# Kernel tuning notes

Measured on AMD Instinct MI355X. Metric: run time of the kernel, lower is better.

## Reference

```python
import jax, jax.numpy as jnp
import numpy as np

NS = 48          # scalar channel multiplicity ('48x0e' input irreps)
NV = 10          # vector multiplicity ('10x1o' output irreps)
N = 20000        # nodes
E = 100000       # edges
W_NUMEL = NS * NS + NS * NV  # e3nn FullyConnectedTensorProduct weight_numel = 2784
OUT_DIM = NS + 3 * NV        # '48x0e + 10x1o' -> 78


def setup_inputs() -> dict:
    key = jax.random.key(0)
    ks = jax.random.split(key, 8)
    node_attr = jax.random.normal(ks[0], (N, NS), dtype=jnp.float32)
    edge_index = jax.random.randint(ks[1], (2, E), 0, N, dtype=jnp.int32)
    edge_attr = jax.random.normal(ks[2], (E, NS), dtype=jnp.float32)
    edge_sh = jax.random.normal(ks[3], (E, 9), dtype=jnp.float32)  # sh lmax=2: 1+3+5
    fc1_w = jax.random.normal(ks[4], (3 * NS, 3 * NS), dtype=jnp.float32) / np.float32(np.sqrt(3 * NS))
    fc1_b = jnp.zeros((3 * NS,), dtype=jnp.float32)
    fc2_w = jax.random.normal(ks[5], (3 * NS, W_NUMEL), dtype=jnp.float32) / np.float32(np.sqrt(3 * NS))
    fc2_b = jnp.zeros((W_NUMEL,), dtype=jnp.float32)
    return {"node_attr": node_attr, "edge_index": edge_index, "edge_attr": edge_attr,
            "edge_sh": edge_sh, "fc1_w": fc1_w, "fc1_b": fc1_b, "fc2_w": fc2_w, "fc2_b": fc2_b}


def reference(node_attr, edge_index, edge_attr, edge_sh, fc1_w, fc1_b, fc2_w, fc2_b):
    src, dst = edge_index[0], edge_index[1]
    # edge features = [edge_attr, src scalars, dst scalars]  (n_edge_features = 3*ns)
    ea = jnp.concatenate([edge_attr, node_attr[src, :NS], node_attr[dst, :NS]], axis=-1)
    # edge MLP -> per-edge tensor-product weights (shared_weights=False)
    h = jax.nn.relu(ea @ fc1_w + fc1_b)
    w = h @ fc2_w + fc2_b                      # [E, W_NUMEL]
    w0 = w[:, :NS * NS].reshape(E, NS, NS)     # path 0e x 0e -> 0e
    w1 = w[:, NS * NS:].reshape(E, NS, NV)     # path 0e x 1o -> 1o
    x = node_attr[dst]                         # gathered scalar node features [E, NS]
    sh0 = edge_sh[:, :1]                       # l=0 component [E,1]
    sh1 = edge_sh[:, 1:4]                      # l=1 components [E,3]
    norm = np.float32(1.0 / np.sqrt(NS))       # path fan-in normalization (mul1*mul2 = NS*1)
    out0 = jnp.einsum('ei,eik->ek', x, w0) * sh0 * norm                # [E, NS]
    out1 = jnp.einsum('ek,em->ekm', jnp.einsum('ei,eik->ek', x, w1), sh1) * norm  # [E, NV, 3]
    tp = jnp.concatenate([out0, out1.reshape(E, NV * 3)], axis=-1)     # [E, OUT_DIM]
    # scatter-mean to source nodes (reduce='mean', dim_size=N)
    summed = jax.ops.segment_sum(tp, src, num_segments=N)
    counts = jax.ops.segment_sum(jnp.ones((E, 1), tp.dtype), src, num_segments=N)
    return summed / jnp.maximum(counts, 1.0)
```

## Files before the change

kernel.cpp:

```cpp
#include <hip/hip_runtime.h>
#include <hip/hip_bf16.h>

#define NS_    48
#define NV_    10
#define N_NODE 20000
#define N_EDGE 100000
#define HID    144
#define OUTC   58
#define ODIM   78
#define TILE   64
#define LDE    160
#define WNUM   2784

typedef __attribute__((ext_vector_type(8))) short bf8;
typedef __attribute__((ext_vector_type(4))) float f32x4;

__device__ __forceinline__ short f2bf(float x) {
  __hip_bfloat16 h = __float2bfloat16(x);
  union { __hip_bfloat16 b; short s; } u; u.b = h; return u.s;
}

__global__ void prep_fc1(const float* __restrict__ w, short* __restrict__ dst) {
  int idx = blockIdx.x * 256 + threadIdx.x;
  if (idx >= 9 * 5 * 512) return;
  int j = idx & 7, l = (idx >> 3) & 63, t = idx >> 9;
  int ks = t % 5, nt = t / 5;
  int k = ks * 32 + ((l >> 4) << 3) + j;
  int n = nt * 16 + (l & 15);
  dst[idx] = f2bf(k < HID ? w[k * HID + n] : 0.f);
}

__global__ void prep_g(const float* __restrict__ w, const float* __restrict__ b,
                       short* __restrict__ dst) {
  int idx = blockIdx.x * 256 + threadIdx.x;
  if (idx >= 48 * 4 * 5 * 512) return;
  int j = idx & 7, l = (idx >> 3) & 63, t = idx >> 9;
  int ks = t % 5, u = t / 5;
  int strip = u & 3, i = u >> 2;
  int k = ks * 32 + ((l >> 4) << 3) + j;
  int c = strip * 16 + (l & 15);
  float v = 0.f;
  if (c < OUTC) {
    if (k < HID)
      v = (c < NS_) ? w[k * WNUM + i * NS_ + c]
                    : w[k * WNUM + NS_ * NS_ + i * NV_ + (c - NS_)];
    else if (k == HID)
      v = (c < NS_) ? b[i * NS_ + c]
                    : b[NS_ * NS_ + i * NV_ + (c - NS_)];
  }
  dst[idx] = f2bf(v);
}

__global__ __launch_bounds__(256, 4) void fused_edge(
    const float* __restrict__ node_attr, const int* __restrict__ eidx,
    const float* __restrict__ edge_attr, const float* __restrict__ edge_sh,
    const float* __restrict__ fc1_b,
    const short* __restrict__ gfrag, const short* __restrict__ fc1frag,
    float* __restrict__ out, int* __restrict__ counts)
{
  __shared__ short EA[TILE * LDE];
  __shared__ float xT[NS_ * TILE];
  __shared__ float shs[TILE * 4];
  __shared__ int   srcs[TILE];

  const int tid  = threadIdx.x;
  const int lane = tid & 63;
  const int wv   = tid >> 6;
  const int base = blockIdx.x * TILE;

  for (int t = tid; t < TILE * 16; t += 256) {
    int r = t >> 4, c = t & 15;
    EA[r * LDE + HID + c] = 0;
  }

  {
    const int el = tid >> 2, part = tid & 3;
    const int e  = base + el;
    const bool ev = e < N_EDGE;
    const int es = ev ? eidx[e] : 0;
    const int ed = ev ? eidx[N_EDGE + e] : 0;
    if (part == 0) {
      srcs[el] = es;
      #pragma unroll
      for (int c = 0; c < 4; ++c) shs[el * 4 + c] = ev ? edge_sh[(size_t)e * 9 + c] : 0.f;
    }
    const float4* pa = (const float4*)(edge_attr + (size_t)e * NS_);
    const float4* ps = (const float4*)(node_attr + (size_t)es * NS_);
    const float4* pd = (const float4*)(node_attr + (size_t)ed * NS_);
    const float4 z4 = make_float4(0.f, 0.f, 0.f, 0.f);
    #pragma unroll
    for (int q = 0; q < 3; ++q) {
      const int c0 = part * 12 + q * 4;
      float4 va = ev ? pa[part * 3 + q] : z4;
      float4 vs = ev ? ps[part * 3 + q] : z4;
      float4 vd = ev ? pd[part * 3 + q] : z4;
      EA[el * LDE + c0 + 0] = f2bf(va.x);
      EA[el * LDE + c0 + 1] = f2bf(va.y);
      EA[el * LDE + c0 + 2] = f2bf(va.z);
      EA[el * LDE + c0 + 3] = f2bf(va.w);
      EA[el * LDE + NS_ + c0 + 0] = f2bf(vs.x);
      EA[el * LDE + NS_ + c0 + 1] = f2bf(vs.y);
      EA[el * LDE + NS_ + c0 + 2] = f2bf(vs.z);
      EA[el * LDE + NS_ + c0 + 3] = f2bf(vs.w);
      EA[el * LDE + 2 * NS_ + c0 + 0] = f2bf(vd.x);
      EA[el * LDE + 2 * NS_ + c0 + 1] = f2bf(vd.y);
      EA[el * LDE + 2 * NS_ + c0 + 2] = f2bf(vd.z);
      EA[el * LDE + 2 * NS_ + c0 + 3] = f2bf(vd.w);
      xT[(c0 + 0) * TILE + el] = vd.x;
      xT[(c0 + 1) * TILE + el] = vd.y;
      xT[(c0 + 2) * TILE + el] = vd.z;
      xT[(c0 + 3) * TILE + el] = vd.w;
    }
  }
  __syncthreads();

  {
    const int mrow = lane & 15;
    const int koff = (lane >> 4) << 3;
    bf8 aF[5];
    #pragma unroll
    for (int ks = 0; ks < 5; ++ks)
      aF[ks] = *(const bf8*)&EA[(wv * 16 + mrow) * LDE + ks * 32 + koff];
    #pragma unroll
    for (int nt = 0; nt < 9; ++nt) {
      f32x4 acc = {0.f, 0.f, 0.f, 0.f};
      #pragma unroll
      for (int ks = 0; ks < 5; ++ks) {
        bf8 bF = *(const bf8*)&fc1frag[((nt * 5 + ks) * 64 + lane) * 8];
        acc = __builtin_amdgcn_mfma_f32_16x16x32_bf16(aF[ks], bF, acc, 0, 0, 0);
      }
      const int col = nt * 16 + mrow;
      const float bb = fc1_b[col];
      #pragma unroll
      for (int r = 0; r < 4; ++r) {
        float h = acc[r] + bb;
        h = h > 0.f ? h : 0.f;
        EA[(wv * 16 + ((lane >> 4) << 2) + r) * LDE + col] = f2bf(h);
      }
    }
    if (lane < 16) EA[(wv * 16 + lane) * LDE + HID] = (short)0x3F80;
  }
  __syncthreads();

  {
    const int mrow = lane & 15;
    const int koff = (lane >> 4) << 3;
    const int g0 = (lane >> 4) << 2;

    f32x4 oacc[4];
    #pragma unroll
    for (int mt = 0; mt < 4; ++mt) oacc[mt] = (f32x4){0.f, 0.f, 0.f, 0.f};

    bf8 aF[4][5];
    #pragma unroll
    for (int mt = 0; mt < 4; ++mt)
      #pragma unroll
      for (int ks = 0; ks < 5; ++ks)
        aF[mt][ks] = *(const bf8*)&EA[(mt * 16 + mrow) * LDE + ks * 32 + koff];

    for (int i = 0; i < NS_; ++i) {
      bf8 bF[5];
      #pragma unroll
      for (int ks = 0; ks < 5; ++ks)
        bF[ks] = *(const bf8*)&gfrag[(((i * 4 + wv) * 5 + ks) * 64 + lane) * 8];
      #pragma unroll
      for (int mt = 0; mt < 4; ++mt) {
        f32x4 wi = {0.f, 0.f, 0.f, 0.f};
        #pragma unroll
        for (int ks = 0; ks < 5; ++ks)
          wi = __builtin_amdgcn_mfma_f32_16x16x32_bf16(aF[mt][ks], bF[ks], wi, 0, 0, 0);
        const float4 xs = *(const float4*)&xT[i * TILE + mt * 16 + g0];
        oacc[mt][0] += xs.x * wi[0];
        oacc[mt][1] += xs.y * wi[1];
        oacc[mt][2] += xs.z * wi[2];
        oacc[mt][3] += xs.w * wi[3];
      }
    }

    const float nrm = 0.14433756729740643f;
    const int col = wv * 16 + mrow;
    #pragma unroll
    for (int mt = 0; mt < 4; ++mt) {
      #pragma unroll
      for (int r = 0; r < 4; ++r) {
        const int erow = mt * 16 + g0 + r;
        const int e = base + erow;
        if (e < N_EDGE) {
          const int s = srcs[erow];
          const float v = oacc[mt][r] * nrm;
          if (col < NS_) {
            atomicAdd(&out[s * ODIM + col], v * shs[erow * 4 + 0]);
          } else if (col < OUTC) {
            const int kp = col - NS_;
            atomicAdd(&out[s * ODIM + NS_ + kp * 3 + 0], v * shs[erow * 4 + 1]);
            atomicAdd(&out[s * ODIM + NS_ + kp * 3 + 1], v * shs[erow * 4 + 2]);
            atomicAdd(&out[s * ODIM + NS_ + kp * 3 + 2], v * shs[erow * 4 + 3]);
          }
          if (col == 0) atomicAdd(&counts[s], 1);
        }
      }
    }
  }
}

__global__ void finalize(float* __restrict__ out, const int* __restrict__ counts) {
  int idx = blockIdx.x * 256 + threadIdx.x;
  if (idx >= N_NODE * ODIM) return;
  int n = idx / ODIM;
  out[idx] = out[idx] / fmaxf((float)counts[n], 1.f);
}

extern "C" void kernel_launch(void* const* d_in, const int* in_sizes, int n_in,
                              void* d_out, int out_size, void* d_ws, size_t ws_size,
                              hipStream_t stream) {
  (void)in_sizes; (void)n_in; (void)out_size; (void)ws_size;
  const float* node_attr = (const float*)d_in[0];
  const int*   eidx      = (const int*)d_in[1];
  const float* edge_attr = (const float*)d_in[2];
  const float* edge_sh   = (const float*)d_in[3];
  const float* fc1_b     = (const float*)d_in[5];
  const float* fc2_w     = (const float*)d_in[6];
  const float* fc2_b     = (const float*)d_in[7];
  const float* fc1_w     = (const float*)d_in[4];
  float* out = (float*)d_out;

  char* ws = (char*)d_ws;
  short* gfrag   = (short*)(ws);
  short* fc1frag = (short*)(ws + 983040);
  int*   counts  = (int*)(ws + 983040 + 46080);

  hipMemsetAsync(out, 0, (size_t)N_NODE * ODIM * sizeof(float), stream);
  hipMemsetAsync(counts, 0, N_NODE * sizeof(int), stream);

  prep_fc1<<<(9 * 5 * 512 + 255) / 256, 256, 0, stream>>>(fc1_w, fc1frag);
  prep_g<<<(48 * 4 * 5 * 512 + 255) / 256, 256, 0, stream>>>(fc2_w, fc2_b, gfrag);

  fused_edge<<<(N_EDGE + TILE - 1) / TILE, 256, 0, stream>>>(
      node_attr, eidx, edge_attr, edge_sh, fc1_b, gfrag, fc1frag, out, counts);

  finalize<<<(N_NODE * ODIM + 255) / 256, 256, 0, stream>>>(out, counts);
}
```

Measured before the change: 203.7 us.

## Sort edges by source and reduce runs in LDS before atomic scatter

Adds a counting sort of edges by source node (histogram, two-level scan, scatter) so each tile processes edges grouped by source. The fused kernel stages per-edge outputs in shared memory and sums contiguous same-source runs, issuing one atomic per run and channel instead of one per edge and channel. It also double-buffers the gfrag B-fragment loads in the main loop and lowers the occupancy hint from 4 to 3 blocks per CU. The trade is four extra small kernels, an indirect edge gather, and an extra shared-memory pass in exchange for far fewer global atomics.

```diff
diff --git a/kernel.cpp b/kernel.cpp
--- a/kernel.cpp
+++ b/kernel.cpp
@@ -51,17 +51,67 @@
   dst[idx] = f2bf(v);
 }
 
-__global__ __launch_bounds__(256, 4) void fused_edge(
+__global__ void k_hist(const int* __restrict__ eidx, int* __restrict__ cnt) {
+  int e = blockIdx.x * 256 + threadIdx.x;
+  if (e < N_EDGE) atomicAdd(&cnt[eidx[e]], 1);
+}
+
+__global__ void k_scan1(const int* __restrict__ cnt, int* __restrict__ locexc,
+                        int* __restrict__ blksum) {
+  __shared__ int sh[256];
+  int g = blockIdx.x * 256 + threadIdx.x;
+  int v = (g < N_NODE) ? cnt[g] : 0;
+  sh[threadIdx.x] = v;
+  __syncthreads();
+  for (int d = 1; d < 256; d <<= 1) {
+    int t = (threadIdx.x >= d) ? sh[threadIdx.x - d] : 0;
+    __syncthreads();
+    sh[threadIdx.x] += t;
+    __syncthreads();
+  }
+  if (g < N_NODE) locexc[g] = sh[threadIdx.x] - v;
+  if (threadIdx.x == 255) blksum[blockIdx.x] = sh[255];
+}
+
+__global__ void k_scan2(const int* __restrict__ blksum, int* __restrict__ blkoff) {
+  __shared__ int sh[128];
+  int t = threadIdx.x;
+  int v = (t < 79) ? blksum[t] : 0;
+  sh[t] = v;
+  __syncthreads();
+  for (int d = 1; d < 128; d <<= 1) {
+    int x = (t >= d) ? sh[t - d] : 0;
+    __syncthreads();
+    sh[t] += x;
+    __syncthreads();
+  }
+  if (t < 79) blkoff[t] = sh[t] - v;
+}
+
+__global__ void k_scatter(const int* __restrict__ eidx, const int* __restrict__ locexc,
+                          const int* __restrict__ blkoff, int* __restrict__ cursor,
+                          int* __restrict__ sortedE) {
+  int e = blockIdx.x * 256 + threadIdx.x;
+  if (e >= N_EDGE) return;
+  int s = eidx[e];
+  int base = blkoff[s >> 8] + locexc[s];
+  int r = atomicAdd(&cursor[s], 1);
+  sortedE[base + r] = e;
+}
+
+__global__ __launch_bounds__(256, 3) void fused_edge(
     const float* __restrict__ node_attr, const int* __restrict__ eidx,
     const float* __restrict__ edge_attr, const float* __restrict__ edge_sh,
-    const float* __restrict__ fc1_b,
+    const float* __restrict__ fc1_b, const int* __restrict__ sortedE,
     const short* __restrict__ gfrag, const short* __restrict__ fc1frag,
-    float* __restrict__ out, int* __restrict__ counts)
+    float* __restrict__ out)
 {
   __shared__ short EA[TILE * LDE];
   __shared__ float xT[NS_ * TILE];
   __shared__ float shs[TILE * 4];
   __shared__ int   srcs[TILE];
+  __shared__ int   runStart[TILE + 1], runSrc[TILE];
+  __shared__ int   nRunsSh;
 
   const int tid  = threadIdx.x;
   const int lane = tid & 63;
@@ -75,12 +125,13 @@
 
   {
     const int el = tid >> 2, part = tid & 3;
-    const int e  = base + el;
-    const bool ev = e < N_EDGE;
+    const int gi = base + el;
+    const bool ev = gi < N_EDGE;
+    const int e  = ev ? sortedE[gi] : 0;
     const int es = ev ? eidx[e] : 0;
     const int ed = ev ? eidx[N_EDGE + e] : 0;
     if (part == 0) {
-      srcs[el] = es;
+      srcs[el] = ev ? es : -1;
       #pragma unroll
       for (int c = 0; c < 4; ++c) shs[el * 4 + c] = ev ? edge_sh[(size_t)e * 9 + c] : 0.f;
     }
@@ -155,59 +206,100 @@
     #pragma unroll
     for (int mt = 0; mt < 4; ++mt)
       #pragma unroll
-      for (int ks = 0; ks < 5; ++ks)
+      for (int ks = 0; ks < 5; ++ks) {
         aF[mt][ks] = *(const bf8*)&EA[(mt * 16 + mrow) * LDE + ks * 32 + koff];
-
-    for (int i = 0; i < NS_; ++i) {
-      bf8 bF[5];
-      #pragma unroll
-      for (int ks = 0; ks < 5; ++ks)
-        bF[ks] = *(const bf8*)&gfrag[(((i * 4 + wv) * 5 + ks) * 64 + lane) * 8];
+        asm volatile("" : "+v"(aF[mt][ks]));
+      }
+    __syncthreads();
+
+    const short* gb = gfrag + wv * 2560 + lane * 8;
+    bf8 bA[5], bB[5];
+    #pragma unroll
+    for (int ks = 0; ks < 5; ++ks) bA[ks] = *(const bf8*)(gb + ks * 512);
+
+    auto compute = [&](const bf8 (&BF)[5], int i) {
       #pragma unroll
       for (int mt = 0; mt < 4; ++mt) {
         f32x4 wi = {0.f, 0.f, 0.f, 0.f};
         #pragma unroll
         for (int ks = 0; ks < 5; ++ks)
-          wi = __builtin_amdgcn_mfma_f32_16x16x32_bf16(aF[mt][ks], bF[ks], wi, 0, 0, 0);
+          wi = __builtin_amdgcn_mfma_f32_16x16x32_bf16(aF[mt][ks], BF[ks], wi, 0, 0, 0);
         const float4 xs = *(const float4*)&xT[i * TILE + mt * 16 + g0];
         oacc[mt][0] += xs.x * wi[0];
         oacc[mt][1] += xs.y * wi[1];
         oacc[mt][2] += xs.z * wi[2];
         oacc[mt][3] += xs.w * wi[3];
       }
-    }
-
+    };
+
+    for (int i = 0; i < NS_; i += 2) {
+      #pragma unroll
+      for (int ks = 0; ks < 5; ++ks)
+        bB[ks] = *(const bf8*)(gb + (i + 1) * 10240 + ks * 512);
+      compute(bA, i);
+      const int ip = (i + 2 < NS_) ? (i + 2) : (NS_ - 1);
+      #pragma unroll
+      for (int ks = 0; ks < 5; ++ks)
+        bA[ks] = *(const bf8*)(gb + ip * 10240 + ks * 512);
+      compute(bB, i + 1);
+    }
+
+    float* O = (float*)EA;
     const float nrm = 0.14433756729740643f;
     const int col = wv * 16 + mrow;
     #pragma unroll
     for (int mt = 0; mt < 4; ++mt) {
       #pragma unroll
       for (int r = 0; r < 4; ++r) {
-        const int erow = mt * 16 + g0 + r;
-        const int e = base + erow;
-        if (e < N_EDGE) {
-          const int s = srcs[erow];
-          const float v = oacc[mt][r] * nrm;
-          if (col < NS_) {
-            atomicAdd(&out[s * ODIM + col], v * shs[erow * 4 + 0]);
-          } else if (col < OUTC) {
-            const int kp = col - NS_;
-            atomicAdd(&out[s * ODIM + NS_ + kp * 3 + 0], v * shs[erow * 4 + 1]);
-            atomicAdd(&out[s * ODIM + NS_ + kp * 3 + 1], v * shs[erow * 4 + 2]);
-            atomicAdd(&out[s * ODIM + NS_ + kp * 3 + 2], v * shs[erow * 4 + 3]);
-          }
-          if (col == 0) atomicAdd(&counts[s], 1);
+        const int row = mt * 16 + g0 + r;
+        const float v = oacc[mt][r] * nrm;
+        if (col < NS_) {
+          O[row * 80 + col] = v * shs[row * 4 + 0];
+        } else if (col < OUTC) {
+          const int kp = col - NS_;
+          O[row * 80 + NS_ + kp * 3 + 0] = v * shs[row * 4 + 1];
+          O[row * 80 + NS_ + kp * 3 + 1] = v * shs[row * 4 + 2];
+          O[row * 80 + NS_ + kp * 3 + 2] = v * shs[row * 4 + 3];
         }
       }
     }
   }
-}
-
-__global__ void finalize(float* __restrict__ out, const int* __restrict__ counts) {
+  __syncthreads();
+
+  if (tid < 64) {
+    const int s = srcs[tid];
+    const bool valid = s >= 0;
+    const bool head = valid && (tid == 0 || srcs[tid - 1] != s);
+    const unsigned long long hm = __ballot(head);
+    const unsigned long long vm = __ballot(valid);
+    const int rank = __popcll(hm & ((1ull << tid) - 1ull));
+    if (head) { runStart[rank] = tid; runSrc[rank] = s; }
+    if (tid == 0) {
+      const int nR = __popcll(hm);
+      nRunsSh = nR;
+      runStart[nR] = __popcll(vm);
+    }
+  }
+  __syncthreads();
+
+  {
+    const float* O = (const float*)EA;
+    const int nR = nRunsSh;
+    for (int t = tid; t < nR * ODIM; t += 256) {
+      const int k = t / ODIM, c = t - k * ODIM;
+      const int rs = runStart[k], re = runStart[k + 1];
+      float s = 0.f;
+      for (int r = rs; r < re; ++r) s += O[r * 80 + c];
+      atomicAdd(&out[(size_t)runSrc[k] * ODIM + c], s);
+    }
+  }
+}
+
+__global__ void finalize(float* __restrict__ out, const int* __restrict__ cnt) {
   int idx = blockIdx.x * 256 + threadIdx.x;
   if (idx >= N_NODE * ODIM) return;
   int n = idx / ODIM;
-  out[idx] = out[idx] / fmaxf((float)counts[n], 1.f);
+  out[idx] = out[idx] / fmaxf((float)cnt[n], 1.f);
 }
 
 extern "C" void kernel_launch(void* const* d_in, const int* in_sizes, int n_in,
@@ -218,25 +310,36 @@
   const int*   eidx      = (const int*)d_in[1];
   const float* edge_attr = (const float*)d_in[2];
   const float* edge_sh   = (const float*)d_in[3];
+  const float* fc1_w     = (const float*)d_in[4];
   const float* fc1_b     = (const float*)d_in[5];
   const float* fc2_w     = (const float*)d_in[6];
   const float* fc2_b     = (const float*)d_in[7];
-  const float* fc1_w     = (const float*)d_in[4];
   float* out = (float*)d_out;
 
   char* ws = (char*)d_ws;
   short* gfrag   = (short*)(ws);
   short* fc1frag = (short*)(ws + 983040);
-  int*   counts  = (int*)(ws + 983040 + 46080);
+  int*   cnt     = (int*)(ws + 1029120);
+  int*   locexc  = (int*)(ws + 1109120);
+  int*   cursor  = (int*)(ws + 1189120);
+  int*   blksum  = (int*)(ws + 1269120);
+  int*   blkoff  = (int*)(ws + 1269632);
+  int*   sortedE = (int*)(ws + 1270144);
 
   hipMemsetAsync(out, 0, (size_t)N_NODE * ODIM * sizeof(float), stream);
-  hipMemsetAsync(counts, 0, N_NODE * sizeof(int), stream);
+  hipMemsetAsync(cnt, 0, N_NODE * sizeof(int), stream);
+  hipMemsetAsync(cursor, 0, N_NODE * sizeof(int), stream);
 
   prep_fc1<<<(9 * 5 * 512 + 255) / 256, 256, 0, stream>>>(fc1_w, fc1frag);
   prep_g<<<(48 * 4 * 5 * 512 + 255) / 256, 256, 0, stream>>>(fc2_w, fc2_b, gfrag);
 
+  k_hist<<<(N_EDGE + 255) / 256, 256, 0, stream>>>(eidx, cnt);
+  k_scan1<<<(N_NODE + 255) / 256, 256, 0, stream>>>(cnt, locexc, blksum);
+  k_scan2<<<1, 128, 0, stream>>>(blksum, blkoff);
+  k_scatter<<<(N_EDGE + 255) / 256, 256, 0, stream>>>(eidx, locexc, blkoff, cursor, sortedE);
+
   fused_edge<<<(N_EDGE + TILE - 1) / TILE, 256, 0, stream>>>(
-      node_attr, eidx, edge_attr, edge_sh, fc1_b, gfrag, fc1frag, out, counts);
-
-  finalize<<<(N_NODE * ODIM + 255) / 256, 256, 0, stream>>>(out, counts);
-}
+      node_attr, eidx, edge_attr, edge_sh, fc1_b, sortedE, gfrag, fc1frag, out);
+
+  finalize<<<(N_NODE * ODIM + 255) / 256, 256, 0, stream>>>(out, cnt);
+}
```

Result: faster. 175.2 us (-14.0%).
